# Optimization experiments

Measured on AMD Instinct MI355X. Metric: run time of the kernel, lower is better.

## Reference

```python
import jax, jax.numpy as jnp
import numpy as np

B, S, HID, H = 8, 128, 256, 4
DH = HID // H
FF = 4 * HID


def setup_inputs() -> dict:
    key = jax.random.key(0)
    ks = jax.random.split(key, 16)
    n = lambda i, shape: jax.random.normal(ks[i], shape, dtype=jnp.float32) * 0.02
    z = lambda shape: jnp.zeros(shape, dtype=jnp.float32)
    return dict(
        x=jax.random.normal(ks[0], (B, S, HID), dtype=jnp.float32),
        attention_mask=jnp.zeros((B, 1, S, S), dtype=jnp.float32),
        Wq=n(1, (HID, HID)), bq=z((HID,)),
        Wk=n(2, (HID, HID)), bk=z((HID,)),
        Wv=n(3, (HID, HID)), bv=z((HID,)),
        order_w=n(4, (2 * DH,)), order_b=z(()),
        dist_w=n(5, (2 * DH,)), dist_b=z(()),
        scalar=jax.random.normal(ks[6], (1,), dtype=jnp.float32),
        AWq=n(7, (HID, HID)), Abq=z((HID,)),
        AWk=n(8, (HID, HID)), Abk=z((HID,)),
        Wd=n(9, (HID, HID)), bd=z((HID,)),
        g1=jnp.ones((HID,), jnp.float32), beta1=z((HID,)),
        W1=n(10, (HID, FF)), b1=z((FF,)),
        W2=n(11, (FF, HID)), b2=z((HID,)),
        g2=jnp.ones((HID,), jnp.float32), beta2=z((HID,)),
    )


def _ln(t, g, b, eps=1e-12):
    m = t.mean(-1, keepdims=True)
    v = ((t - m) ** 2).mean(-1, keepdims=True)
    return (t - m) / jnp.sqrt(v + eps) * g + b


def _heads(t):
    # [B,S,HID] -> [B,H,S,DH]
    return t.reshape(B, S, H, DH).transpose(0, 2, 1, 3)


def reference(x, attention_mask, Wq, bq, Wk, bk, Wv, bv, order_w, order_b,
              dist_w, dist_b, scalar, AWq, Abq, AWk, Abk, Wd, bd,
              g1, beta1, W1, b1, W2, b2, g2, beta2):
    inv = 1.0 / jnp.sqrt(jnp.float32(DH))
    q = x @ Wq + bq
    k = x @ Wk + bk
    v = x @ Wv + bv
    qh, kh, vh = _heads(q), _heads(k), _heads(v)
    scores = jnp.einsum('bhqd,bhkd->bhqk', qh, kh)  # [B,H,S,S]

    # order/distance affines on concat(q_i, k_j): Linear(2*DH,1) decomposes into
    # per-token projections summed via broadcast (same math, no [B,H,S,S,2*DH] tensor)
    pr_order = jax.nn.sigmoid((qh @ order_w[:DH])[..., :, None]
                              + (kh @ order_w[DH:])[..., None, :] + order_b)
    gd_order = jnp.triu(jnp.ones((S, S), jnp.float32), k=1)
    err_order = (jnp.log(pr_order + 1e-24) * gd_order
                 + jnp.log(1.0 - pr_order + 1e-24) * (1.0 - gd_order))

    idx = jnp.arange(S)
    gd_dist = jnp.log(jnp.abs(idx[None, :] - idx[:, None]).astype(jnp.float32) + 1.0)
    pr_dist = ((qh @ dist_w[:DH])[..., :, None]
               + (kh @ dist_w[DH:])[..., None, :] + dist_b)
    err_dist = -jnp.square(gd_dist - pr_dist) * jnp.square(scalar[0]) * 0.5

    rich_scores = scores + err_order + err_dist
    softm = lambda s: jax.nn.softmax(s * inv + attention_mask, axis=-1)
    rich_probs = softm(rich_scores)
    origin_probs = softm(scores)

    # rich/calibrated combine ('fixed'): softmax(origin + 0.5 * rich)
    combined = jax.nn.softmax(origin_probs + 0.5 * rich_probs, axis=-1)

    # two-level attack attention on transformed mixed q/k
    aq, ak = _heads(q @ AWq + Abq), _heads(k @ AWk + Abk)
    attack_probs = softm(jnp.einsum('bhqd,bhkd->bhqk', aq, ak))
    final_probs = jax.nn.softmax(combined + 0.5 * attack_probs, axis=-1)

    ctx = jnp.einsum('bhqk,bhkd->bhqd', final_probs, vh)
    ctx = ctx.transpose(0, 2, 1, 3).reshape(B, S, HID)
    h = _ln(ctx @ Wd + bd + x, g1, beta1)
    f = jax.nn.gelu(h @ W1 + b1, approximate=False) @ W2 + b2
    return _ln(f + h, g2, beta2)
```

## Files before the change

### kernel.cpp

```cpp
#include <hip/hip_runtime.h>
#include <math.h>

#define B_  8
#define S_  128
#define HID_ 256
#define H_  4
#define DH_ 64
#define FF_ 1024
#define M_  (B_ * S_)

typedef _Float16 half_t;
typedef __attribute__((ext_vector_type(8))) _Float16 half8;
typedef __attribute__((ext_vector_type(4))) float floatx4;

enum { EP_F32 = 0, EP_F16 = 1, EP_F16B = 2, EP_GELU = 3, EP_PROJ = 4 };

__device__ __forceinline__ floatx4 mfma16(half8 a, half8 b, floatx4 c) {
    return __builtin_amdgcn_mfma_f32_16x16x32_f16(a, b, c, 0, 0, 0);
}

__device__ __forceinline__ float qred_sum(float v) {
#pragma unroll
    for (int o = 1; o < 16; o <<= 1) v += __shfl_xor(v, o, 64);
    return v;
}
__device__ __forceinline__ void sm8(float (&v)[8]) {
    float s = 0.f;
#pragma unroll
    for (int j = 0; j < 8; ++j) { v[j] = __expf(v[j]); s += v[j]; }
    s = qred_sum(s);
    float r = 1.f / s;
#pragma unroll
    for (int j = 0; j < 8; ++j) v[j] *= r;
}

template<int EPI, int KLEN>
__device__ __forceinline__ void mgemm(
    half8 (&Asf)[2][4][64], half8 (&Bsf)[2][4][64],
    const half_t* __restrict__ A, int ldA,
    const half_t* __restrict__ Bt, int ldB,
    int m0, int n0,
    const float* __restrict__ bias,
    float* __restrict__ Cf, half_t* __restrict__ Ch, int ldC,
    const float* __restrict__ pw1, const float* __restrict__ pw2,
    float* __restrict__ po1, float* __restrict__ po2, int hsel,
    int crb, int cnb, int tidp)
{
    constexpr int kt = KLEN >> 5;
    const int w = tidp >> 6, l = tidp & 63;
    const int sr = tidp >> 2;
    const int sq = tidp & 3;
    const int sdst = (sr & 15) | (sq << 4);
    const int smt = sr >> 4;
    const half_t* Ap = A + (size_t)(m0 + sr) * ldA + sq * 8;
    const half_t* Bp = Bt + (size_t)(n0 + sr) * ldB + sq * 8;

    half8 ra[kt], rb[kt];
#pragma unroll
    for (int t = 0; t < kt; ++t) {
        ra[t] = *(const half8*)(Ap + t * 32);
        rb[t] = *(const half8*)(Bp + t * 32);
    }

    floatx4 zero = {0.f, 0.f, 0.f, 0.f};
    floatx4 acc[4] = {zero, zero, zero, zero};

    Asf[0][smt][sdst] = ra[0];
    Bsf[0][smt][sdst] = rb[0];
    __syncthreads();
#pragma unroll
    for (int t = 0; t < kt; ++t) {
        const int buf = t & 1;
        half8 a = Asf[buf][w][l];
        acc[0] = mfma16(a, Bsf[buf][0][l], acc[0]);
        acc[1] = mfma16(a, Bsf[buf][1][l], acc[1]);
        acc[2] = mfma16(a, Bsf[buf][2][l], acc[2]);
        acc[3] = mfma16(a, Bsf[buf][3][l], acc[3]);
        if (t + 1 < kt) {
            Asf[buf ^ 1][smt][sdst] = ra[t + 1];
            Bsf[buf ^ 1][smt][sdst] = rb[t + 1];
            __syncthreads();
        }
    }

    const int quad = l >> 4, lc = l & 15;
    const int rowb = m0 + w * 16 + quad * 4;
    float bvv[4] = {0.f, 0.f, 0.f, 0.f};
    if (EPI >= EP_F16B) {
#pragma unroll
        for (int nt = 0; nt < 4; ++nt) bvv[nt] = bias[n0 + nt * 16 + lc];
    }
    float pw1v[4], pw2v[4];
    if (EPI == EP_PROJ) {
#pragma unroll
        for (int nt = 0; nt < 4; ++nt) {
            pw1v[nt] = pw1[nt * 16 + lc];
            pw2v[nt] = pw2[nt * 16 + lc];
        }
    }
#pragma unroll
    for (int rr = 0; rr < 4; ++rr) {
        float ov[4];
#pragma unroll
        for (int nt = 0; nt < 4; ++nt) {
            float o = acc[nt][rr];
            if (EPI >= EP_F16B) o += bvv[nt];
            if (EPI == EP_GELU) o = 0.5f * o * (1.f + erff(o * 0.70710678118654752f));
            ov[nt] = o;
            const size_t ci = (size_t)(rowb + rr - crb) * ldC + (n0 - cnb) + nt * 16 + lc;
            if (EPI == EP_F32) Cf[ci] = o;
            else Ch[ci] = (half_t)o;
        }
        if (EPI == EP_PROJ) {
            float po = ov[0] * pw1v[0] + ov[1] * pw1v[1] + ov[2] * pw1v[2] + ov[3] * pw1v[3];
            float pd = ov[0] * pw2v[0] + ov[1] * pw2v[1] + ov[2] * pw2v[2] + ov[3] * pw2v[3];
#pragma unroll
            for (int off = 1; off < 16; off <<= 1) {
                po += __shfl_xor(po, off, 64);
                pd += __shfl_xor(pd, off, 64);
            }
            if (lc == 0) {
                const int m = rowb + rr;
                const int idx = ((m >> 7) * H_ + hsel) * S_ + (m & 127);
                po1[idx] = po;
                po2[idx] = pd;
            }
        }
    }
}

__global__ __launch_bounds__(256) void prep_kernel(
    const float* __restrict__ x,
    const float* __restrict__ Wq, const float* __restrict__ Wk,
    const float* __restrict__ Wv, const float* __restrict__ Wd,
    const float* __restrict__ AWq, const float* __restrict__ AWk,
    const float* __restrict__ W1, const float* __restrict__ W2,
    half_t* __restrict__ x16, half_t* __restrict__ WqT, half_t* __restrict__ WkT,
    half_t* __restrict__ WvT, half_t* __restrict__ WdT,
    half_t* __restrict__ AWqT, half_t* __restrict__ AWkT,
    half_t* __restrict__ W1T, half_t* __restrict__ W2T)
{
    __shared__ half_t tl[64][72];
    const int tid = threadIdx.x;
    const int j = blockIdx.x;
    if (j < 256) {
        const int base = j * 1024 + tid * 4;
        float4 vv = *(const float4*)(x + base);
        x16[base + 0] = (half_t)vv.x;
        x16[base + 1] = (half_t)vv.y;
        x16[base + 2] = (half_t)vv.z;
        x16[base + 3] = (half_t)vv.w;
        return;
    }
    int t = j - 256;
    const float* src; half_t* dst; int K, N, k0, n0;
    if (t < 96) {
        int m = t >> 4, q = t & 15;
        const float* ins[6] = {Wq, Wk, Wv, Wd, AWq, AWk};
        half_t* outs[6] = {WqT, WkT, WvT, WdT, AWqT, AWkT};
        src = ins[m]; dst = outs[m]; K = 256; N = 256;
        k0 = (q & 3) * 64; n0 = (q >> 2) * 64;
    } else if (t < 160) {
        int q = t - 96; src = W1; dst = W1T; K = 256; N = 1024;
        k0 = (q & 3) * 64; n0 = (q >> 2) * 64;
    } else {
        int q = t - 160; src = W2; dst = W2T; K = 1024; N = 256;
        k0 = (q >> 2) * 64; n0 = (q & 3) * 64;
    }
    const int r = tid >> 2, c0 = (tid & 3) * 16;
#pragma unroll 4
    for (int i = 0; i < 16; ++i)
        tl[c0 + i][r] = (half_t)src[(size_t)(k0 + r) * N + n0 + c0 + i];
    __syncthreads();
#pragma unroll 4
    for (int i = 0; i < 16; ++i)
        dst[(size_t)(n0 + r) * K + k0 + c0 + i] = tl[r][c0 + i];
}

__global__ __launch_bounds__(256) void qkv_kernel(
    const half_t* __restrict__ x16,
    const half_t* __restrict__ WqT, const float* __restrict__ bq,
    const half_t* __restrict__ WkT, const float* __restrict__ bk,
    const half_t* __restrict__ WvT, const float* __restrict__ bv,
    const float* __restrict__ order_w, const float* __restrict__ dist_w,
    half_t* __restrict__ q16, half_t* __restrict__ k16, half_t* __restrict__ v16,
    float* __restrict__ qoA, float* __restrict__ qdA,
    float* __restrict__ koA, float* __restrict__ kdA)
{
    __shared__ half8 Asf[2][4][64], Bsf[2][4][64];
    const int j = blockIdx.x;
    const int z = j >> 6, q = j & 63;
    const int m0 = (q >> 2) * 64, n0 = (q & 3) * 64, bx = q & 3;
    if (z == 0)
        mgemm<EP_PROJ, 256>(Asf, Bsf, x16, HID_, WqT, HID_, m0, n0,
                            bq, nullptr, q16, HID_, order_w, dist_w, qoA, qdA, bx,
                            0, 0, threadIdx.x);
    else if (z == 1)
        mgemm<EP_PROJ, 256>(Asf, Bsf, x16, HID_, WkT, HID_, m0, n0,
                            bk, nullptr, k16, HID_, order_w + DH_, dist_w + DH_,
                            koA, kdA, bx, 0, 0, threadIdx.x);
    else
        mgemm<EP_F16B, 256>(Asf, Bsf, x16, HID_, WvT, HID_, m0, n0,
                            bv, nullptr, v16, HID_, nullptr, nullptr, nullptr, nullptr, 0,
                            0, 0, threadIdx.x);
}

struct AttnSmem {
    union {
        struct { half8 Asf[2][2][4][64]; half8 Bsf[2][2][4][64]; } g;
        struct { half_t Vt[64][136]; half8 Kf[2][8][64];
                 half_t Pm[8][16][136]; } a;
    } u;
    half_t aq_s[128][72];
    half_t ak_s[128][72];
};

__global__ __launch_bounds__(512) void attn_kernel(
    const half_t* __restrict__ q16, const half_t* __restrict__ k16,
    const half_t* __restrict__ v16,
    const half_t* __restrict__ AWqT, const half_t* __restrict__ AWkT,
    const float* __restrict__ Abq, const float* __restrict__ Abk,
    const float* __restrict__ qoA, const float* __restrict__ qdA,
    const float* __restrict__ koA, const float* __restrict__ kdA,
    const float* __restrict__ mask,
    const float* __restrict__ order_b_p, const float* __restrict__ dist_b_p,
    const float* __restrict__ scalar_p,
    half_t* __restrict__ ctx16)
{
    __shared__ AttnSmem sm;
    const int bh = blockIdx.x;
    const int b = bh >> 2, h = bh & 3;
    const int tid = threadIdx.x;
    const int half_id = tid >> 8, ltid = tid & 255;
    const int w = tid >> 6, l = tid & 63;
    const int quad = l >> 4, lc = l & 15;
    const size_t hoff = (size_t)b * S_ * HID_ + (size_t)h * DH_;
    const floatx4 zero = {0.f, 0.f, 0.f, 0.f};

    {
        const half_t* Asrc = half_id ? (k16 + (size_t)b * S_ * HID_)
                                     : (q16 + (size_t)b * S_ * HID_);
        const half_t* WT   = half_id ? AWkT : AWqT;
        const float*  bb   = half_id ? Abk : Abq;
        half_t* dst        = half_id ? &sm.ak_s[0][0] : &sm.aq_s[0][0];
        mgemm<EP_F16B, 256>(sm.u.g.Asf[half_id], sm.u.g.Bsf[half_id],
                            Asrc, HID_, WT, HID_, 0, h * DH_,
                            bb, nullptr, dst, 72, nullptr, nullptr, nullptr, nullptr, 0,
                            0, h * DH_, ltid);
        mgemm<EP_F16B, 256>(sm.u.g.Asf[half_id], sm.u.g.Bsf[half_id],
                            Asrc, HID_, WT, HID_, 64, h * DH_,
                            bb, nullptr, dst, 72, nullptr, nullptr, nullptr, nullptr, 0,
                            0, h * DH_, ltid);
    }
    __syncthreads();

#pragma unroll
    for (int u = 0; u < 2; ++u) {
        int idx = u * 512 + tid;
        int jj = idx >> 3, c = idx & 7;
        size_t g = hoff + (size_t)jj * HID_ + c * 8;
        int kt2 = c >> 2, jt = jj >> 4, sl = (jj & 15) | ((c & 3) << 4);
        sm.u.a.Kf[kt2][jt][sl] = *(const half8*)(k16 + g);
    }
#pragma unroll
    for (int u = 0; u < 2; ++u) {
        int idx = u * 512 + tid;
        int jj = idx >> 3, c = idx & 7;
        half8 vv = *(const half8*)(v16 + hoff + (size_t)jj * HID_ + c * 8);
#pragma unroll
        for (int e = 0; e < 8; ++e) sm.u.a.Vt[c * 8 + e][jj] = vv[e];
    }
    __syncthreads();

    const float ob = order_b_p[0], db = dist_b_p[0];
    const float scl = scalar_p[0];
    const float s2 = scl * scl;
    const float inv = 0.125f;
    float kov[8], kdv[8];
#pragma unroll
    for (int jt = 0; jt < 8; ++jt) {
        kov[jt] = koA[bh * S_ + jt * 16 + lc];
        kdv[jt] = kdA[bh * S_ + jt * 16 + lc];
    }

    const int rt = w;
    half8 qf[2], aqf[2];
#pragma unroll
    for (int kt = 0; kt < 2; ++kt) {
        qf[kt]  = *(const half8*)(q16 + hoff + (size_t)(rt * 16 + lc) * HID_
                                  + kt * 32 + quad * 8);
        aqf[kt] = *(const half8*)&sm.aq_s[rt * 16 + lc][kt * 32 + quad * 8];
    }
    floatx4 accS[8], accA[8];
#pragma unroll
    for (int jt = 0; jt < 8; ++jt) { accS[jt] = zero; accA[jt] = zero; }
#pragma unroll
    for (int kt = 0; kt < 2; ++kt) {
#pragma unroll
        for (int jt = 0; jt < 8; ++jt) {
            accS[jt] = mfma16(qf[kt], sm.u.a.Kf[kt][jt][l], accS[jt]);
            half8 bfr = *(const half8*)&sm.ak_s[jt * 16 + lc][kt * 32 + quad * 8];
            accA[jt] = mfma16(aqf[kt], bfr, accA[jt]);
        }
    }
#pragma unroll
    for (int reg = 0; reg < 4; ++reg) {
        const int il = quad * 4 + reg;
        const int i  = rt * 16 + il;
        float qo = qoA[bh * S_ + i], qd = qdA[bh * S_ + i];
        const float* mrow = mask + ((size_t)(b * S_ + i)) * S_;
        float mk[8], lg[8], as_[8];
#pragma unroll
        for (int jt = 0; jt < 8; ++jt) {
            mk[jt] = mrow[jt * 16 + lc];
            lg[jt] = accS[jt][reg];
            as_[jt] = accA[jt][reg];
        }
        float p0[8];
#pragma unroll
        for (int jt = 0; jt < 8; ++jt) p0[jt] = lg[jt] * inv + mk[jt];
        sm8(p0);
        float p1[8];
#pragma unroll
        for (int jt = 0; jt < 8; ++jt) {
            int j = jt * 16 + lc;
            float pr = 1.f / (1.f + __expf(-(qo + kov[jt] + ob)));
            float sel = (j > i) ? pr : 1.f - pr;
            float erro = __logf(sel + 1e-24f);
            float gd = __logf(fabsf((float)(j - i)) + 1.f);
            float dd = gd - (qd + kdv[jt] + db);
            p1[jt] = (lg[jt] + erro - 0.5f * dd * dd * s2) * inv + mk[jt];
        }
        sm8(p1);
#pragma unroll
        for (int jt = 0; jt < 8; ++jt) p0[jt] += 0.5f * p1[jt];
        sm8(p0);
#pragma unroll
        for (int jt = 0; jt < 8; ++jt) p1[jt] = as_[jt] * inv + mk[jt];
        sm8(p1);
#pragma unroll
        for (int jt = 0; jt < 8; ++jt) p0[jt] += 0.5f * p1[jt];
        sm8(p0);
#pragma unroll
        for (int jt = 0; jt < 8; ++jt) sm.u.a.Pm[w][il][jt * 16 + lc] = (half_t)p0[jt];
    }
    half8 pa_[4];
#pragma unroll
    for (int kt = 0; kt < 4; ++kt)
        pa_[kt] = *(const half8*)&sm.u.a.Pm[w][lc][kt * 32 + quad * 8];
    floatx4 apv[4] = {zero, zero, zero, zero};
#pragma unroll
    for (int nt = 0; nt < 4; ++nt) {
#pragma unroll
        for (int kt = 0; kt < 4; ++kt) {
            half8 vf = *(const half8*)&sm.u.a.Vt[nt * 16 + lc][kt * 32 + quad * 8];
            apv[nt] = mfma16(pa_[kt], vf, apv[nt]);
        }
    }
#pragma unroll
    for (int nt = 0; nt < 4; ++nt) {
#pragma unroll
        for (int reg = 0; reg < 4; ++reg) {
            int i = rt * 16 + quad * 4 + reg;
            ctx16[hoff + (size_t)i * HID_ + nt * 16 + lc] = (half_t)apv[nt][reg];
        }
    }
}

struct TailSmem {
    half8 Af[8][64];
    float hS[16][257];
    half_t h16L[16][264];
    half_t f116L[16][1032];
};

__global__ __launch_bounds__(512) void tail_kernel(
    const half_t* __restrict__ ctx16, const half_t* __restrict__ WdT,
    const float* __restrict__ x, const float* __restrict__ bd,
    const float* __restrict__ g1, const float* __restrict__ beta1,
    const half_t* __restrict__ W1T, const float* __restrict__ b1,
    const half_t* __restrict__ W2T, const float* __restrict__ b2,
    const float* __restrict__ g2, const float* __restrict__ beta2,
    float* __restrict__ out)
{
    __shared__ TailSmem sm;
    const int tid = threadIdx.x;
    const int r0 = blockIdx.x * 16;
    const int w = tid >> 6, l = tid & 63;
    const int quad = l >> 4, lc = l & 15;
    const floatx4 zero = {0.f, 0.f, 0.f, 0.f};

    {
        int row = tid >> 5, c = tid & 31;
        sm.Af[c >> 2][row | ((c & 3) << 4)] =
            *(const half8*)(ctx16 + (size_t)(r0 + row) * HID_ + c * 8);
    }
    __syncthreads();

    {
        const int n0 = w * 32;
        half8 bw[8][2];
#pragma unroll
        for (int kt = 0; kt < 8; ++kt)
#pragma unroll
            for (int nt = 0; nt < 2; ++nt)
                bw[kt][nt] = *(const half8*)(WdT + (size_t)(n0 + nt * 16 + lc) * HID_
                                             + kt * 32 + quad * 8);
        floatx4 acc[2] = {zero, zero};
#pragma unroll
        for (int kt = 0; kt < 8; ++kt) {
            half8 a = sm.Af[kt][l];
            acc[0] = mfma16(a, bw[kt][0], acc[0]);
            acc[1] = mfma16(a, bw[kt][1], acc[1]);
        }
#pragma unroll
        for (int nt = 0; nt < 2; ++nt)
#pragma unroll
            for (int rr = 0; rr < 4; ++rr) {
                int row = quad * 4 + rr, col = n0 + nt * 16 + lc;
                sm.hS[row][col] = acc[nt][rr] + bd[col]
                                + x[(size_t)(r0 + row) * HID_ + col];
            }
    }
    __syncthreads();

    {
        const int row = tid >> 5, jj = tid & 31;
        float s = 0.f;
#pragma unroll
        for (int i = 0; i < 8; ++i) s += sm.hS[row][i * 32 + jj];
#pragma unroll
        for (int o = 1; o < 32; o <<= 1) s += __shfl_xor(s, o, 64);
        float mean = s * (1.f / 256.f);
        float vs = 0.f;
#pragma unroll
        for (int i = 0; i < 8; ++i) { float d = sm.hS[row][i * 32 + jj] - mean; vs += d * d; }
#pragma unroll
        for (int o = 1; o < 32; o <<= 1) vs += __shfl_xor(vs, o, 64);
        float rs = rsqrtf(vs * (1.f / 256.f) + 1e-12f);
#pragma unroll
        for (int i = 0; i < 8; ++i) {
            int col = i * 32 + jj;
            float v = (sm.hS[row][col] - mean) * rs * g1[col] + beta1[col];
            sm.hS[row][col] = v;
            sm.h16L[row][col] = (half_t)v;
        }
    }
    __syncthreads();

#pragma unroll
    for (int nb = 0; nb < 2; ++nb) {
        const int n0 = w * 128 + nb * 64;
        floatx4 acc[4] = {zero, zero, zero, zero};
        half8 bw[2][4][4];
#pragma unroll
        for (int kt = 0; kt < 4; ++kt)
#pragma unroll
            for (int nt = 0; nt < 4; ++nt)
                bw[0][kt][nt] = *(const half8*)(W1T + (size_t)(n0 + nt * 16 + lc) * HID_
                                                + kt * 32 + quad * 8);
#pragma unroll
        for (int c = 0; c < 2; ++c) {
            if (c == 0) {
#pragma unroll
                for (int kt = 0; kt < 4; ++kt)
#pragma unroll
                    for (int nt = 0; nt < 4; ++nt)
                        bw[1][kt][nt] = *(const half8*)(W1T
                            + (size_t)(n0 + nt * 16 + lc) * HID_ + (4 + kt) * 32 + quad * 8);
            }
#pragma unroll
            for (int kt = 0; kt < 4; ++kt) {
                half8 a = *(const half8*)&sm.h16L[l & 15][(c * 4 + kt) * 32 + quad * 8];
#pragma unroll
                for (int nt = 0; nt < 4; ++nt)
                    acc[nt] = mfma16(a, bw[c][kt][nt], acc[nt]);
            }
        }
#pragma unroll
        for (int nt = 0; nt < 4; ++nt)
#pragma unroll
            for (int rr = 0; rr < 4; ++rr) {
                int row = quad * 4 + rr, col = n0 + nt * 16 + lc;
                float o = acc[nt][rr] + b1[col];
                o = 0.5f * o * (1.f + erff(o * 0.70710678118654752f));
                sm.f116L[row][col] = (half_t)o;
            }
    }
    __syncthreads();

    {
        const int n0 = w * 32;
        floatx4 acc[2] = {zero, zero};
        half8 bw[2][4][2];
#pragma unroll
        for (int kt = 0; kt < 4; ++kt)
#pragma unroll
            for (int nt = 0; nt < 2; ++nt)
                bw[0][kt][nt] = *(const half8*)(W2T + (size_t)(n0 + nt * 16 + lc) * FF_
                                                + kt * 32 + quad * 8);
#pragma unroll
        for (int c = 0; c < 8; ++c) {
            if (c < 7) {
#pragma unroll
                for (int kt = 0; kt < 4; ++kt)
#pragma unroll
                    for (int nt = 0; nt < 2; ++nt)
                        bw[(c + 1) & 1][kt][nt] = *(const half8*)(W2T
                            + (size_t)(n0 + nt * 16 + lc) * FF_ + ((c + 1) * 4 + kt) * 32 + quad * 8);
            }
#pragma unroll
            for (int kt = 0; kt < 4; ++kt) {
                half8 a = *(const half8*)&sm.f116L[l & 15][(c * 4 + kt) * 32 + quad * 8];
#pragma unroll
                for (int nt = 0; nt < 2; ++nt)
                    acc[nt] = mfma16(a, bw[c & 1][kt][nt], acc[nt]);
            }
        }
#pragma unroll
        for (int nt = 0; nt < 2; ++nt)
#pragma unroll
            for (int rr = 0; rr < 4; ++rr) {
                int row = quad * 4 + rr, col = n0 + nt * 16 + lc;
                sm.hS[row][col] = acc[nt][rr] + b2[col] + sm.hS[row][col];
            }
    }
    __syncthreads();

    {
        const int row = tid >> 5, jj = tid & 31;
        float s = 0.f;
#pragma unroll
        for (int i = 0; i < 8; ++i) s += sm.hS[row][i * 32 + jj];
#pragma unroll
        for (int o = 1; o < 32; o <<= 1) s += __shfl_xor(s, o, 64);
        float mean = s * (1.f / 256.f);
        float vs = 0.f;
#pragma unroll
        for (int i = 0; i < 8; ++i) { float d = sm.hS[row][i * 32 + jj] - mean; vs += d * d; }
#pragma unroll
        for (int o = 1; o < 32; o <<= 1) vs += __shfl_xor(vs, o, 64);
        float rs = rsqrtf(vs * (1.f / 256.f) + 1e-12f);
#pragma unroll
        for (int i = 0; i < 8; ++i) {
            int col = i * 32 + jj;
            out[(size_t)(r0 + row) * HID_ + col] =
                (sm.hS[row][col] - mean) * rs * g2[col] + beta2[col];
        }
    }
}

extern "C" void kernel_launch(void* const* d_in, const int* in_sizes, int n_in,
                              void* d_out, int out_size, void* d_ws, size_t ws_size,
                              hipStream_t stream) {
    const float* x        = (const float*)d_in[0];
    const float* mask     = (const float*)d_in[1];
    const float* Wq       = (const float*)d_in[2];
    const float* bq       = (const float*)d_in[3];
    const float* Wk       = (const float*)d_in[4];
    const float* bk       = (const float*)d_in[5];
    const float* Wv       = (const float*)d_in[6];
    const float* bv       = (const float*)d_in[7];
    const float* order_w  = (const float*)d_in[8];
    const float* order_b  = (const float*)d_in[9];
    const float* dist_w   = (const float*)d_in[10];
    const float* dist_b   = (const float*)d_in[11];
    const float* scalar   = (const float*)d_in[12];
    const float* AWq      = (const float*)d_in[13];
    const float* Abq      = (const float*)d_in[14];
    const float* AWk      = (const float*)d_in[15];
    const float* Abk      = (const float*)d_in[16];
    const float* Wd       = (const float*)d_in[17];
    const float* bd       = (const float*)d_in[18];
    const float* g1       = (const float*)d_in[19];
    const float* beta1    = (const float*)d_in[20];
    const float* W1       = (const float*)d_in[21];
    const float* b1       = (const float*)d_in[22];
    const float* W2       = (const float*)d_in[23];
    const float* b2       = (const float*)d_in[24];
    const float* g2       = (const float*)d_in[25];
    const float* beta2    = (const float*)d_in[26];

    float* ws = (float*)d_ws;
    size_t off = 0;
    auto ahf = [&](size_t nh) { half_t* p = (half_t*)(ws + off); off += nh / 2; return p; };
    auto afl = [&](size_t n) { float* p = ws + off; off += n; return p; };

    half_t* x16   = ahf(M_ * HID_);
    half_t* WqT   = ahf(HID_ * HID_);
    half_t* WkT   = ahf(HID_ * HID_);
    half_t* WvT   = ahf(HID_ * HID_);
    half_t* WdT   = ahf(HID_ * HID_);
    half_t* AWqT  = ahf(HID_ * HID_);
    half_t* AWkT  = ahf(HID_ * HID_);
    half_t* W1T   = ahf(HID_ * FF_);
    half_t* W2T   = ahf(HID_ * FF_);
    half_t* q16   = ahf(M_ * HID_);
    half_t* k16   = ahf(M_ * HID_);
    half_t* v16   = ahf(M_ * HID_);
    half_t* ctx16 = ahf(M_ * HID_);
    float* qoA  = afl(B_ * H_ * S_);
    float* qdA  = afl(B_ * H_ * S_);
    float* koA  = afl(B_ * H_ * S_);
    float* kdA  = afl(B_ * H_ * S_);

    prep_kernel<<<480, 256, 0, stream>>>(
        x, Wq, Wk, Wv, Wd, AWq, AWk, W1, W2,
        x16, WqT, WkT, WvT, WdT, AWqT, AWkT, W1T, W2T);
    qkv_kernel<<<192, 256, 0, stream>>>(
        x16, WqT, bq, WkT, bk, WvT, bv, order_w, dist_w,
        q16, k16, v16, qoA, qdA, koA, kdA);
    attn_kernel<<<32, 512, 0, stream>>>(
        q16, k16, v16, AWqT, AWkT, Abq, Abk,
        qoA, qdA, koA, kdA, mask, order_b, dist_b, scalar, ctx16);
    tail_kernel<<<64, 512, 0, stream>>>(
        ctx16, WdT, x, bd, g1, beta1, W1T, b1, W2T, b2, g2, beta2, (float*)d_out);
}
```

Before: 178.6 us.

## Fold attack projections into composed weights and split attention across more blocks

```diff
diff --git a/kernel.cpp b/kernel.cpp
--- a/kernel.cpp
+++ b/kernel.cpp
@@ -22,6 +22,11 @@
 __device__ __forceinline__ float qred_sum(float v) {
 #pragma unroll
     for (int o = 1; o < 16; o <<= 1) v += __shfl_xor(v, o, 64);
+    return v;
+}
+__device__ __forceinline__ float wred64(float v) {
+#pragma unroll
+    for (int o = 1; o < 64; o <<= 1) v += __shfl_xor(v, o, 64);
     return v;
 }
 __device__ __forceinline__ void sm8(float (&v)[8]) {
@@ -44,7 +49,7 @@
     float* __restrict__ Cf, half_t* __restrict__ Ch, int ldC,
     const float* __restrict__ pw1, const float* __restrict__ pw2,
     float* __restrict__ po1, float* __restrict__ po2, int hsel,
-    int crb, int cnb, int tidp)
+    int tidp)
 {
     constexpr int kt = KLEN >> 5;
     const int w = tidp >> 6, l = tidp & 63;
@@ -105,9 +110,8 @@
         for (int nt = 0; nt < 4; ++nt) {
             float o = acc[nt][rr];
             if (EPI >= EP_F16B) o += bvv[nt];
-            if (EPI == EP_GELU) o = 0.5f * o * (1.f + erff(o * 0.70710678118654752f));
             ov[nt] = o;
-            const size_t ci = (size_t)(rowb + rr - crb) * ldC + (n0 - cnb) + nt * 16 + lc;
+            const size_t ci = (size_t)(rowb + rr) * ldC + n0 + nt * 16 + lc;
             if (EPI == EP_F32) Cf[ci] = o;
             else Ch[ci] = (half_t)o;
         }
@@ -133,16 +137,24 @@
     const float* __restrict__ x,
     const float* __restrict__ Wq, const float* __restrict__ Wk,
     const float* __restrict__ Wv, const float* __restrict__ Wd,
+    const float* __restrict__ W1, const float* __restrict__ W2,
     const float* __restrict__ AWq, const float* __restrict__ AWk,
-    const float* __restrict__ W1, const float* __restrict__ W2,
+    const float* __restrict__ bq, const float* __restrict__ bk,
+    const float* __restrict__ Abq, const float* __restrict__ Abk,
     half_t* __restrict__ x16, half_t* __restrict__ WqT, half_t* __restrict__ WkT,
     half_t* __restrict__ WvT, half_t* __restrict__ WdT,
-    half_t* __restrict__ AWqT, half_t* __restrict__ AWkT,
-    half_t* __restrict__ W1T, half_t* __restrict__ W2T)
+    half_t* __restrict__ W1T, half_t* __restrict__ W2T,
+    half_t* __restrict__ WcqT, half_t* __restrict__ WckT,
+    float* __restrict__ bcq, float* __restrict__ bck)
 {
-    __shared__ half_t tl[64][72];
+    __shared__ union {
+        half_t tl[64][72];
+        struct { half_t As[64][264]; half_t Bs[64][264]; } c;
+        float red[4][64];
+    } sm;
     const int tid = threadIdx.x;
     const int j = blockIdx.x;
+
     if (j < 256) {
         const int base = j * 1024 + tid * 4;
         float4 vv = *(const float4*)(x + base);
@@ -152,38 +164,117 @@
         x16[base + 3] = (half_t)vv.w;
         return;
     }
-    int t = j - 256;
-    const float* src; half_t* dst; int K, N, k0, n0;
-    if (t < 96) {
-        int m = t >> 4, q = t & 15;
-        const float* ins[6] = {Wq, Wk, Wv, Wd, AWq, AWk};
-        half_t* outs[6] = {WqT, WkT, WvT, WdT, AWqT, AWkT};
-        src = ins[m]; dst = outs[m]; K = 256; N = 256;
-        k0 = (q & 3) * 64; n0 = (q >> 2) * 64;
-    } else if (t < 160) {
-        int q = t - 96; src = W1; dst = W1T; K = 256; N = 1024;
-        k0 = (q & 3) * 64; n0 = (q >> 2) * 64;
-    } else {
-        int q = t - 160; src = W2; dst = W2T; K = 1024; N = 256;
-        k0 = (q >> 2) * 64; n0 = (q & 3) * 64;
-    }
-    const int r = tid >> 2, c0 = (tid & 3) * 16;
+    if (j < 448) {
+        int t = j - 256;
+        const float* src; half_t* dst; int K, N, k0, n0;
+        if (t < 64) {
+            int m = t >> 4, q = t & 15;
+            const float* ins[4] = {Wq, Wk, Wv, Wd};
+            half_t* outs[4] = {WqT, WkT, WvT, WdT};
+            src = ins[m]; dst = outs[m]; K = 256; N = 256;
+            k0 = (q & 3) * 64; n0 = (q >> 2) * 64;
+        } else if (t < 128) {
+            int q = t - 64; src = W1; dst = W1T; K = 256; N = 1024;
+            k0 = (q & 3) * 64; n0 = (q >> 2) * 64;
+        } else {
+            int q = t - 128; src = W2; dst = W2T; K = 1024; N = 256;
+            k0 = (q >> 2) * 64; n0 = (q & 3) * 64;
+        }
+        const int r = tid >> 2, c0 = (tid & 3) * 16;
 #pragma unroll 4
-    for (int i = 0; i < 16; ++i)
-        tl[c0 + i][r] = (half_t)src[(size_t)(k0 + r) * N + n0 + c0 + i];
-    __syncthreads();
+        for (int i = 0; i < 16; ++i)
+            sm.tl[c0 + i][r] = (half_t)src[(size_t)(k0 + r) * N + n0 + c0 + i];
+        __syncthreads();
 #pragma unroll 4
-    for (int i = 0; i < 16; ++i)
-        dst[(size_t)(n0 + r) * K + k0 + c0 + i] = tl[r][c0 + i];
-}
-
-__global__ __launch_bounds__(256) void qkv_kernel(
+        for (int i = 0; i < 16; ++i)
+            dst[(size_t)(n0 + r) * K + k0 + c0 + i] = sm.tl[r][c0 + i];
+        return;
+    }
+    if (j < 480) {
+        int t = j - 448;
+        const int z = t >> 4, q = t & 15;
+        const int m0 = (q >> 2) * 64, n0 = (q & 3) * 64;
+        const float* AW = z ? AWk : AWq;
+        const float* W  = z ? Wk : Wq;
+        half_t* C       = z ? WckT : WcqT;
+        {
+            const float* srcA = AW + (size_t)tid * HID_ + m0;
+#pragma unroll 4
+            for (int i = 0; i < 16; ++i) {
+                float4 v = *(const float4*)(srcA + i * 4);
+                sm.c.As[i * 4 + 0][tid] = (half_t)v.x;
+                sm.c.As[i * 4 + 1][tid] = (half_t)v.y;
+                sm.c.As[i * 4 + 2][tid] = (half_t)v.z;
+                sm.c.As[i * 4 + 3][tid] = (half_t)v.w;
+            }
+        }
+        {
+            const int bn = tid >> 2, bc = (tid & 3) * 64;
+            const float* srcB = W + (size_t)(n0 + bn) * HID_ + bc;
+            half_t* dstB = &sm.c.Bs[bn][bc];
+#pragma unroll 4
+            for (int i = 0; i < 16; ++i) {
+                float4 v = *(const float4*)(srcB + i * 4);
+                dstB[i * 4 + 0] = (half_t)v.x;
+                dstB[i * 4 + 1] = (half_t)v.y;
+                dstB[i * 4 + 2] = (half_t)v.z;
+                dstB[i * 4 + 3] = (half_t)v.w;
+            }
+        }
+        __syncthreads();
+        const int w = tid >> 6, l = tid & 63;
+        const int quad = l >> 4, lc = l & 15;
+        const floatx4 zero = {0.f, 0.f, 0.f, 0.f};
+        floatx4 acc[4] = {zero, zero, zero, zero};
+#pragma unroll
+        for (int kt = 0; kt < 8; ++kt) {
+            half8 a = *(const half8*)&sm.c.As[w * 16 + lc][kt * 32 + quad * 8];
+#pragma unroll
+            for (int nt = 0; nt < 4; ++nt) {
+                half8 b = *(const half8*)&sm.c.Bs[nt * 16 + lc][kt * 32 + quad * 8];
+                acc[nt] = mfma16(a, b, acc[nt]);
+            }
+        }
+#pragma unroll
+        for (int nt = 0; nt < 4; ++nt)
+#pragma unroll
+            for (int rr = 0; rr < 4; ++rr)
+                C[(size_t)(m0 + w * 16 + quad * 4 + rr) * HID_ + n0 + nt * 16 + lc] =
+                    (half_t)acc[nt][rr];
+        return;
+    }
+    {
+        int t = j - 480;
+        const int z = t >> 2, xb = t & 3;
+        const float* bsrc = z ? bk : bq;
+        const float* AW   = z ? AWk : AWq;
+        const float* Ab   = z ? Abk : Abq;
+        float* bco        = z ? bck : bcq;
+        int l = tid & 63, kc = tid >> 6;
+        int n = xb * 64 + l;
+        float p = 0.f;
+#pragma unroll 8
+        for (int kk = 0; kk < 64; ++kk) {
+            int k = kc * 64 + kk;
+            p = fmaf(bsrc[k], AW[(size_t)k * HID_ + n], p);
+        }
+        sm.red[kc][l] = p;
+        __syncthreads();
+        if (kc == 0)
+            bco[n] = sm.red[0][l] + sm.red[1][l] + sm.red[2][l] + sm.red[3][l] + Ab[n];
+    }
+}
+
+__global__ __launch_bounds__(256) void xgemm5(
     const half_t* __restrict__ x16,
     const half_t* __restrict__ WqT, const float* __restrict__ bq,
     const half_t* __restrict__ WkT, const float* __restrict__ bk,
     const half_t* __restrict__ WvT, const float* __restrict__ bv,
+    const half_t* __restrict__ WcqT, const float* __restrict__ bcq,
+    const half_t* __restrict__ WckT, const float* __restrict__ bck,
     const float* __restrict__ order_w, const float* __restrict__ dist_w,
     half_t* __restrict__ q16, half_t* __restrict__ k16, half_t* __restrict__ v16,
+    half_t* __restrict__ aq16, half_t* __restrict__ ak16,
     float* __restrict__ qoA, float* __restrict__ qdA,
     float* __restrict__ koA, float* __restrict__ kdA)
 {
@@ -194,32 +285,29 @@
     if (z == 0)
         mgemm<EP_PROJ, 256>(Asf, Bsf, x16, HID_, WqT, HID_, m0, n0,
                             bq, nullptr, q16, HID_, order_w, dist_w, qoA, qdA, bx,
-                            0, 0, threadIdx.x);
+                            threadIdx.x);
     else if (z == 1)
         mgemm<EP_PROJ, 256>(Asf, Bsf, x16, HID_, WkT, HID_, m0, n0,
                             bk, nullptr, k16, HID_, order_w + DH_, dist_w + DH_,
-                            koA, kdA, bx, 0, 0, threadIdx.x);
-    else
+                            koA, kdA, bx, threadIdx.x);
+    else if (z == 2)
         mgemm<EP_F16B, 256>(Asf, Bsf, x16, HID_, WvT, HID_, m0, n0,
                             bv, nullptr, v16, HID_, nullptr, nullptr, nullptr, nullptr, 0,
-                            0, 0, threadIdx.x);
-}
-
-struct AttnSmem {
-    union {
-        struct { half8 Asf[2][2][4][64]; half8 Bsf[2][2][4][64]; } g;
-        struct { half_t Vt[64][136]; half8 Kf[2][8][64];
-                 half_t Pm[8][16][136]; } a;
-    } u;
-    half_t aq_s[128][72];
-    half_t ak_s[128][72];
-};
-
-__global__ __launch_bounds__(512) void attn_kernel(
+                            threadIdx.x);
+    else if (z == 3)
+        mgemm<EP_F16B, 256>(Asf, Bsf, x16, HID_, WcqT, HID_, m0, n0,
+                            bcq, nullptr, aq16, HID_, nullptr, nullptr, nullptr, nullptr, 0,
+                            threadIdx.x);
+    else
+        mgemm<EP_F16B, 256>(Asf, Bsf, x16, HID_, WckT, HID_, m0, n0,
+                            bck, nullptr, ak16, HID_, nullptr, nullptr, nullptr, nullptr, 0,
+                            threadIdx.x);
+}
+
+__global__ __launch_bounds__(64) void attn_kernel(
     const half_t* __restrict__ q16, const half_t* __restrict__ k16,
-    const half_t* __restrict__ v16,
-    const half_t* __restrict__ AWqT, const half_t* __restrict__ AWkT,
-    const float* __restrict__ Abq, const float* __restrict__ Abk,
+    const half_t* __restrict__ v16, const half_t* __restrict__ aq16,
+    const half_t* __restrict__ ak16,
     const float* __restrict__ qoA, const float* __restrict__ qdA,
     const float* __restrict__ koA, const float* __restrict__ kdA,
     const float* __restrict__ mask,
@@ -227,50 +315,54 @@
     const float* __restrict__ scalar_p,
     half_t* __restrict__ ctx16)
 {
-    __shared__ AttnSmem sm;
-    const int bh = blockIdx.x;
+    __shared__ half8 Kf[2][8][64], AKf[2][8][64];
+    __shared__ half_t Vt[64][136];
+    __shared__ half_t Pm[16][136];
+
+    const int l = threadIdx.x;
+    const int quad = l >> 4, lc = l & 15;
+    const int bh = blockIdx.x >> 3, rt = blockIdx.x & 7;
     const int b = bh >> 2, h = bh & 3;
-    const int tid = threadIdx.x;
-    const int half_id = tid >> 8, ltid = tid & 255;
-    const int w = tid >> 6, l = tid & 63;
-    const int quad = l >> 4, lc = l & 15;
     const size_t hoff = (size_t)b * S_ * HID_ + (size_t)h * DH_;
-    const floatx4 zero = {0.f, 0.f, 0.f, 0.f};
-
-    {
-        const half_t* Asrc = half_id ? (k16 + (size_t)b * S_ * HID_)
-                                     : (q16 + (size_t)b * S_ * HID_);
-        const half_t* WT   = half_id ? AWkT : AWqT;
-        const float*  bb   = half_id ? Abk : Abq;
-        half_t* dst        = half_id ? &sm.ak_s[0][0] : &sm.aq_s[0][0];
-        mgemm<EP_F16B, 256>(sm.u.g.Asf[half_id], sm.u.g.Bsf[half_id],
-                            Asrc, HID_, WT, HID_, 0, h * DH_,
-                            bb, nullptr, dst, 72, nullptr, nullptr, nullptr, nullptr, 0,
-                            0, h * DH_, ltid);
-        mgemm<EP_F16B, 256>(sm.u.g.Asf[half_id], sm.u.g.Bsf[half_id],
-                            Asrc, HID_, WT, HID_, 64, h * DH_,
-                            bb, nullptr, dst, 72, nullptr, nullptr, nullptr, nullptr, 0,
-                            0, h * DH_, ltid);
-    }
-    __syncthreads();
-
-#pragma unroll
-    for (int u = 0; u < 2; ++u) {
-        int idx = u * 512 + tid;
-        int jj = idx >> 3, c = idx & 7;
-        size_t g = hoff + (size_t)jj * HID_ + c * 8;
-        int kt2 = c >> 2, jt = jj >> 4, sl = (jj & 15) | ((c & 3) << 4);
-        sm.u.a.Kf[kt2][jt][sl] = *(const half8*)(k16 + g);
-    }
-#pragma unroll
-    for (int u = 0; u < 2; ++u) {
-        int idx = u * 512 + tid;
-        int jj = idx >> 3, c = idx & 7;
-        half8 vv = *(const half8*)(v16 + hoff + (size_t)jj * HID_ + c * 8);
-#pragma unroll
-        for (int e = 0; e < 8; ++e) sm.u.a.Vt[c * 8 + e][jj] = vv[e];
-    }
-    __syncthreads();
+
+#pragma unroll
+    for (int u = 0; u < 16; ++u) {
+        int idx = u * 64 + l;
+        int j = idx >> 3, c = idx & 7;
+        size_t g = hoff + (size_t)j * HID_ + c * 8;
+        int kt = c >> 2, jt = j >> 4, sl = (j & 15) | ((c & 3) << 4);
+        Kf[kt][jt][sl]  = *(const half8*)(k16 + g);
+        AKf[kt][jt][sl] = *(const half8*)(ak16 + g);
+    }
+#pragma unroll
+    for (int u = 0; u < 16; ++u) {
+        int j = (u >> 3) * 64 + l;
+        int c = u & 7;
+        half8 vv = *(const half8*)(v16 + hoff + (size_t)j * HID_ + c * 8);
+#pragma unroll
+        for (int e = 0; e < 8; ++e) Vt[c * 8 + e][j] = vv[e];
+    }
+    __syncthreads();
+
+    half8 qf[2], aqf[2];
+#pragma unroll
+    for (int kt = 0; kt < 2; ++kt) {
+        size_t g = hoff + (size_t)(rt * 16 + lc) * HID_ + kt * 32 + quad * 8;
+        qf[kt]  = *(const half8*)(q16 + g);
+        aqf[kt] = *(const half8*)(aq16 + g);
+    }
+    floatx4 zero = {0.f, 0.f, 0.f, 0.f};
+    floatx4 accS[8], accA[8];
+#pragma unroll
+    for (int jt = 0; jt < 8; ++jt) { accS[jt] = zero; accA[jt] = zero; }
+#pragma unroll
+    for (int kt = 0; kt < 2; ++kt) {
+#pragma unroll
+        for (int jt = 0; jt < 8; ++jt) {
+            accS[jt] = mfma16(qf[kt], Kf[kt][jt][l], accS[jt]);
+            accA[jt] = mfma16(aqf[kt], AKf[kt][jt][l], accA[jt]);
+        }
+    }
 
     const float ob = order_b_p[0], db = dist_b_p[0];
     const float scl = scalar_p[0];
@@ -281,27 +373,6 @@
     for (int jt = 0; jt < 8; ++jt) {
         kov[jt] = koA[bh * S_ + jt * 16 + lc];
         kdv[jt] = kdA[bh * S_ + jt * 16 + lc];
-    }
-
-    const int rt = w;
-    half8 qf[2], aqf[2];
-#pragma unroll
-    for (int kt = 0; kt < 2; ++kt) {
-        qf[kt]  = *(const half8*)(q16 + hoff + (size_t)(rt * 16 + lc) * HID_
-                                  + kt * 32 + quad * 8);
-        aqf[kt] = *(const half8*)&sm.aq_s[rt * 16 + lc][kt * 32 + quad * 8];
-    }
-    floatx4 accS[8], accA[8];
-#pragma unroll
-    for (int jt = 0; jt < 8; ++jt) { accS[jt] = zero; accA[jt] = zero; }
-#pragma unroll
-    for (int kt = 0; kt < 2; ++kt) {
-#pragma unroll
-        for (int jt = 0; jt < 8; ++jt) {
-            accS[jt] = mfma16(qf[kt], sm.u.a.Kf[kt][jt][l], accS[jt]);
-            half8 bfr = *(const half8*)&sm.ak_s[jt * 16 + lc][kt * 32 + quad * 8];
-            accA[jt] = mfma16(aqf[kt], bfr, accA[jt]);
-        }
     }
 #pragma unroll
     for (int reg = 0; reg < 4; ++reg) {
@@ -342,18 +413,22 @@
         for (int jt = 0; jt < 8; ++jt) p0[jt] += 0.5f * p1[jt];
         sm8(p0);
 #pragma unroll
-        for (int jt = 0; jt < 8; ++jt) sm.u.a.Pm[w][il][jt * 16 + lc] = (half_t)p0[jt];
-    }
+        for (int jt = 0; jt < 8; ++jt) Pm[il][jt * 16 + lc] = (half_t)p0[jt];
+    }
+    __syncthreads();
+
     half8 pa_[4];
 #pragma unroll
     for (int kt = 0; kt < 4; ++kt)
-        pa_[kt] = *(const half8*)&sm.u.a.Pm[w][lc][kt * 32 + quad * 8];
-    floatx4 apv[4] = {zero, zero, zero, zero};
+        pa_[kt] = *(const half8*)&Pm[lc][kt * 32 + quad * 8];
+    floatx4 apv[4];
+#pragma unroll
+    for (int nt = 0; nt < 4; ++nt) apv[nt] = zero;
 #pragma unroll
     for (int nt = 0; nt < 4; ++nt) {
 #pragma unroll
         for (int kt = 0; kt < 4; ++kt) {
-            half8 vf = *(const half8*)&sm.u.a.Vt[nt * 16 + lc][kt * 32 + quad * 8];
+            half8 vf = *(const half8*)&Vt[nt * 16 + lc][kt * 32 + quad * 8];
             apv[nt] = mfma16(pa_[kt], vf, apv[nt]);
         }
     }
@@ -369,9 +444,9 @@
 
 struct TailSmem {
     half8 Af[8][64];
-    float hS[16][257];
-    half_t h16L[16][264];
-    half_t f116L[16][1032];
+    float hS[8][257];
+    half_t h16L[8][264];
+    half_t f116L[8][1032];
 };
 
 __global__ __launch_bounds__(512) void tail_kernel(
@@ -385,7 +460,7 @@
 {
     __shared__ TailSmem sm;
     const int tid = threadIdx.x;
-    const int r0 = blockIdx.x * 16;
+    const int r0 = blockIdx.x * 8;
     const int w = tid >> 6, l = tid & 63;
     const int quad = l >> 4, lc = l & 15;
     const floatx4 zero = {0.f, 0.f, 0.f, 0.f};
@@ -393,7 +468,7 @@
     {
         int row = tid >> 5, c = tid & 31;
         sm.Af[c >> 2][row | ((c & 3) << 4)] =
-            *(const half8*)(ctx16 + (size_t)(r0 + row) * HID_ + c * 8);
+            *(const half8*)(ctx16 + (size_t)(r0 + (row & 7)) * HID_ + c * 8);
     }
     __syncthreads();
 
@@ -413,34 +488,34 @@
             acc[0] = mfma16(a, bw[kt][0], acc[0]);
             acc[1] = mfma16(a, bw[kt][1], acc[1]);
         }
-#pragma unroll
-        for (int nt = 0; nt < 2; ++nt)
-#pragma unroll
-            for (int rr = 0; rr < 4; ++rr) {
-                int row = quad * 4 + rr, col = n0 + nt * 16 + lc;
-                sm.hS[row][col] = acc[nt][rr] + bd[col]
-                                + x[(size_t)(r0 + row) * HID_ + col];
-            }
+        if (quad < 2) {
+#pragma unroll
+            for (int nt = 0; nt < 2; ++nt)
+#pragma unroll
+                for (int rr = 0; rr < 4; ++rr) {
+                    int row = quad * 4 + rr, col = n0 + nt * 16 + lc;
+                    sm.hS[row][col] = acc[nt][rr] + bd[col]
+                                    + x[(size_t)(r0 + row) * HID_ + col];
+                }
+        }
     }
     __syncthreads();
 
     {
-        const int row = tid >> 5, jj = tid & 31;
+        const int row = tid >> 6, jj = tid & 63;
         float s = 0.f;
 #pragma unroll
-        for (int i = 0; i < 8; ++i) s += sm.hS[row][i * 32 + jj];
-#pragma unroll
-        for (int o = 1; o < 32; o <<= 1) s += __shfl_xor(s, o, 64);
+        for (int i = 0; i < 4; ++i) s += sm.hS[row][i * 64 + jj];
+        s = wred64(s);
         float mean = s * (1.f / 256.f);
         float vs = 0.f;
 #pragma unroll
-        for (int i = 0; i < 8; ++i) { float d = sm.hS[row][i * 32 + jj] - mean; vs += d * d; }
-#pragma unroll
-        for (int o = 1; o < 32; o <<= 1) vs += __shfl_xor(vs, o, 64);
+        for (int i = 0; i < 4; ++i) { float d = sm.hS[row][i * 64 + jj] - mean; vs += d * d; }
+        vs = wred64(vs);
         float rs = rsqrtf(vs * (1.f / 256.f) + 1e-12f);
 #pragma unroll
-        for (int i = 0; i < 8; ++i) {
-            int col = i * 32 + jj;
+        for (int i = 0; i < 4; ++i) {
+            int col = i * 64 + jj;
             float v = (sm.hS[row][col] - mean) * rs * g1[col] + beta1[col];
             sm.hS[row][col] = v;
             sm.h16L[row][col] = (half_t)v;
@@ -471,21 +546,23 @@
             }
 #pragma unroll
             for (int kt = 0; kt < 4; ++kt) {
-                half8 a = *(const half8*)&sm.h16L[l & 15][(c * 4 + kt) * 32 + quad * 8];
+                half8 a = *(const half8*)&sm.h16L[l & 7][(c * 4 + kt) * 32 + quad * 8];
 #pragma unroll
                 for (int nt = 0; nt < 4; ++nt)
                     acc[nt] = mfma16(a, bw[c][kt][nt], acc[nt]);
             }
         }
-#pragma unroll
-        for (int nt = 0; nt < 4; ++nt)
-#pragma unroll
-            for (int rr = 0; rr < 4; ++rr) {
-                int row = quad * 4 + rr, col = n0 + nt * 16 + lc;
-                float o = acc[nt][rr] + b1[col];
-                o = 0.5f * o * (1.f + erff(o * 0.70710678118654752f));
-                sm.f116L[row][col] = (half_t)o;
-            }
+        if (quad < 2) {
+#pragma unroll
+            for (int nt = 0; nt < 4; ++nt)
+#pragma unroll
+                for (int rr = 0; rr < 4; ++rr) {
+                    int row = quad * 4 + rr, col = n0 + nt * 16 + lc;
+                    float o = acc[nt][rr] + b1[col];
+                    o = 0.5f * o * (1.f + erff(o * 0.70710678118654752f));
+                    sm.f116L[row][col] = (half_t)o;
+                }
+        }
     }
     __syncthreads();
 
@@ -511,39 +588,39 @@
             }
 #pragma unroll
             for (int kt = 0; kt < 4; ++kt) {
-                half8 a = *(const half8*)&sm.f116L[l & 15][(c * 4 + kt) * 32 + quad * 8];
+                half8 a = *(const half8*)&sm.f116L[l & 7][(c * 4 + kt) * 32 + quad * 8];
 #pragma unroll
                 for (int nt = 0; nt < 2; ++nt)
                     acc[nt] = mfma16(a, bw[c & 1][kt][nt], acc[nt]);
             }
         }
-#pragma unroll
-        for (int nt = 0; nt < 2; ++nt)
-#pragma unroll
-            for (int rr = 0; rr < 4; ++rr) {
-                int row = quad * 4 + rr, col = n0 + nt * 16 + lc;
-                sm.hS[row][col] = acc[nt][rr] + b2[col] + sm.hS[row][col];
-            }
+        if (quad < 2) {
+#pragma unroll
+            for (int nt = 0; nt < 2; ++nt)
+#pragma unroll
+                for (int rr = 0; rr < 4; ++rr) {
+                    int row = quad * 4 + rr, col = n0 + nt * 16 + lc;
+                    sm.hS[row][col] = acc[nt][rr] + b2[col] + sm.hS[row][col];
+                }
+        }
     }
     __syncthreads();
 
     {
-        const int row = tid >> 5, jj = tid & 31;
+        const int row = tid >> 6, jj = tid & 63;
         float s = 0.f;
 #pragma unroll
-        for (int i = 0; i < 8; ++i) s += sm.hS[row][i * 32 + jj];
-#pragma unroll
-        for (int o = 1; o < 32; o <<= 1) s += __shfl_xor(s, o, 64);
+        for (int i = 0; i < 4; ++i) s += sm.hS[row][i * 64 + jj];
+        s = wred64(s);
         float mean = s * (1.f / 256.f);
         float vs = 0.f;
 #pragma unroll
-        for (int i = 0; i < 8; ++i) { float d = sm.hS[row][i * 32 + jj] - mean; vs += d * d; }
-#pragma unroll
-        for (int o = 1; o < 32; o <<= 1) vs += __shfl_xor(vs, o, 64);
+        for (int i = 0; i < 4; ++i) { float d = sm.hS[row][i * 64 + jj] - mean; vs += d * d; }
+        vs = wred64(vs);
         float rs = rsqrtf(vs * (1.f / 256.f) + 1e-12f);
 #pragma unroll
-        for (int i = 0; i < 8; ++i) {
-            int col = i * 32 + jj;
+        for (int i = 0; i < 4; ++i) {
+            int col = i * 64 + jj;
             out[(size_t)(r0 + row) * HID_ + col] =
                 (sm.hS[row][col] - mean) * rs * g2[col] + beta2[col];
         }
@@ -591,28 +668,32 @@
     half_t* WkT   = ahf(HID_ * HID_);
     half_t* WvT   = ahf(HID_ * HID_);
     half_t* WdT   = ahf(HID_ * HID_);
-    half_t* AWqT  = ahf(HID_ * HID_);
-    half_t* AWkT  = ahf(HID_ * HID_);
     half_t* W1T   = ahf(HID_ * FF_);
     half_t* W2T   = ahf(HID_ * FF_);
+    half_t* WcqT  = ahf(HID_ * HID_);
+    half_t* WckT  = ahf(HID_ * HID_);
     half_t* q16   = ahf(M_ * HID_);
     half_t* k16   = ahf(M_ * HID_);
     half_t* v16   = ahf(M_ * HID_);
+    half_t* aq16  = ahf(M_ * HID_);
+    half_t* ak16  = ahf(M_ * HID_);
     half_t* ctx16 = ahf(M_ * HID_);
+    float* bcq  = afl(256);
+    float* bck  = afl(256);
     float* qoA  = afl(B_ * H_ * S_);
     float* qdA  = afl(B_ * H_ * S_);
     float* koA  = afl(B_ * H_ * S_);
     float* kdA  = afl(B_ * H_ * S_);
 
-    prep_kernel<<<480, 256, 0, stream>>>(
-        x, Wq, Wk, Wv, Wd, AWq, AWk, W1, W2,
-        x16, WqT, WkT, WvT, WdT, AWqT, AWkT, W1T, W2T);
-    qkv_kernel<<<192, 256, 0, stream>>>(
-        x16, WqT, bq, WkT, bk, WvT, bv, order_w, dist_w,
-        q16, k16, v16, qoA, qdA, koA, kdA);
-    attn_kernel<<<32, 512, 0, stream>>>(
-        q16, k16, v16, AWqT, AWkT, Abq, Abk,
-        qoA, qdA, koA, kdA, mask, order_b, dist_b, scalar, ctx16);
-    tail_kernel<<<64, 512, 0, stream>>>(
+    prep_kernel<<<488, 256, 0, stream>>>(
+        x, Wq, Wk, Wv, Wd, W1, W2, AWq, AWk, bq, bk, Abq, Abk,
+        x16, WqT, WkT, WvT, WdT, W1T, W2T, WcqT, WckT, bcq, bck);
+    xgemm5<<<320, 256, 0, stream>>>(
+        x16, WqT, bq, WkT, bk, WvT, bv, WcqT, bcq, WckT, bck, order_w, dist_w,
+        q16, k16, v16, aq16, ak16, qoA, qdA, koA, kdA);
+    attn_kernel<<<256, 64, 0, stream>>>(
+        q16, k16, v16, aq16, ak16, qoA, qdA, koA, kdA,
+        mask, order_b, dist_b, scalar, ctx16);
+    tail_kernel<<<128, 512, 0, stream>>>(
         ctx16, WdT, x, bd, g1, beta1, W1T, b1, W2T, b2, g2, beta2, (float*)d_out);
 }
```

After: 171.0 us. -4.2%, faster.
